# Kernel tuning notes

Hardware: AMD Instinct MI355X
Metric: run time of the kernel (lower is better)

## Reference

```python
import jax, jax.numpy as jnp
import numpy as np
import math

B, T, H, L, N = 8, 256, 1024, 6, 16
S = 3 * T          # interleaved (rtg, state, action) tokens
D = H // N
STATE_DIM, ACT_DIM, MAX_TSTEP, FF = 1024, 64, 4096, 4 * H
EPS = 1e-5


def _ln(x, g, b):
    m = jnp.mean(x, axis=-1, keepdims=True)
    v = jnp.var(x, axis=-1, keepdims=True)
    return (x - m) * jax.lax.rsqrt(v + EPS) * g + b


def setup_inputs() -> dict:
    key = jax.random.key(0)
    ks = jax.random.split(key, 32)
    sc = 0.02
    inp = {
        'timesteps': jax.random.randint(ks[0], (B, T), 0, MAX_TSTEP),
        'states': jax.random.randint(ks[1], (B, T), 0, STATE_DIM),
        'actions': jax.random.randint(ks[2], (B, T), 0, ACT_DIM),
        'returns_to_go': jax.random.normal(ks[3], (B, T, 1), jnp.float32),
        # embeddings
        'Wt': jax.random.normal(ks[4], (MAX_TSTEP, H), jnp.float32) * sc,
        'Ws': jax.random.normal(ks[5], (STATE_DIM, H), jnp.float32) * sc,
        'Wa': jax.random.normal(ks[6], (ACT_DIM, H), jnp.float32) * sc,
        'Wr': jax.random.normal(ks[7], (1, H), jnp.float32) * sc,
        'br': jnp.zeros((H,), jnp.float32),
        'lng': jnp.ones((H,), jnp.float32), 'lnb': jnp.zeros((H,), jnp.float32),
        # per-layer stacked params (weights stored [in,out]: y = x @ W + b)
        'Wq': jax.random.normal(ks[8], (L, H, H), jnp.float32) * sc,
        'bq': jnp.zeros((L, H), jnp.float32),
        'Wk': jax.random.normal(ks[9], (L, H, H), jnp.float32) * sc,
        'bk': jnp.zeros((L, H), jnp.float32),
        'Wv': jax.random.normal(ks[10], (L, H, H), jnp.float32) * sc,
        'bv': jnp.zeros((L, H), jnp.float32),
        'Wp': jax.random.normal(ks[11], (L, H, H), jnp.float32) * sc,
        'bp': jnp.zeros((L, H), jnp.float32),
        'W1': jax.random.normal(ks[12], (L, H, FF), jnp.float32) * sc,
        'b1': jnp.zeros((L, FF), jnp.float32),
        'W2': jax.random.normal(ks[13], (L, FF, H), jnp.float32) * sc,
        'b2': jnp.zeros((L, H), jnp.float32),
        'ln1g': jnp.ones((L, H), jnp.float32), 'ln1b': jnp.zeros((L, H), jnp.float32),
        'ln2g': jnp.ones((L, H), jnp.float32), 'ln2b': jnp.zeros((L, H), jnp.float32),
        # heads
        'Wrtg': jax.random.normal(ks[14], (H, 1), jnp.float32) * sc,
        'brtg': jnp.zeros((1,), jnp.float32),
        'Wst': jax.random.normal(ks[15], (H, STATE_DIM), jnp.float32) * sc,
        'bst': jnp.zeros((STATE_DIM,), jnp.float32),
        'Wac': jax.random.normal(ks[16], (H, ACT_DIM), jnp.float32) * sc,
        'bac': jnp.zeros((ACT_DIM,), jnp.float32),
    }
    return inp


def _attn(x, Wq, bq, Wk, bk, Wv, bv, Wp, bp, mask):
    q = (x @ Wq + bq).reshape(B, S, N, D)
    k = (x @ Wk + bk).reshape(B, S, N, D)
    v = (x @ Wv + bv).reshape(B, S, N, D)
    scores = jnp.einsum('bqhd,bkhd->bhqk', q, k) / math.sqrt(D)
    scores = jnp.where(mask, scores, -jnp.inf)
    p = jax.nn.softmax(scores, axis=-1)
    o = jnp.einsum('bhqk,bkhd->bqhd', p, v).reshape(B, S, H)
    return o @ Wp + bp


def _forward(timesteps, states, actions, returns_to_go, Wt, Ws, Wa, Wr, br,
             lng, lnb, Wq, bq, Wk, bk, Wv, bv, Wp, bp, W1, b1, W2, b2,
             ln1g, ln1b, ln2g, ln2b, Wrtg, brtg, Wst, bst, Wac, bac):
    te = Wt[timesteps]                         # [B,T,H]
    se = Ws[states] + te
    ae = Wa[actions] + te
    re = returns_to_go @ Wr + br + te
    # stack(dim=1).permute(0,2,1,3).reshape -> interleave (rtg, state, action)
    h = jnp.stack([re, se, ae], axis=2).reshape(B, S, H)
    h = _ln(h, lng, lnb)
    mask = jnp.tril(jnp.ones((S, S), bool))[None, None]
    for l in range(L):
        h = h + _attn(h, Wq[l], bq[l], Wk[l], bk[l], Wv[l], bv[l], Wp[l], bp[l], mask)
        h = _ln(h, ln1g[l], ln1b[l])
        h = h + (jax.nn.gelu(h @ W1[l] + b1[l], approximate=False) @ W2[l] + b2[l])
        h = _ln(h, ln2g[l], ln2b[l])
    h = h.reshape(B, 3, T, H)                  # as in the source (contiguous chunks)
    rtg_preds = h[:, 2] @ Wrtg + brtg
    state_preds = h[:, 2] @ Wst + bst
    action_preds = h[:, 1] @ Wac + bac         # discrete actions -> no tanh
    return (state_preds, action_preds, rtg_preds)


def reference(timesteps, states, actions, returns_to_go, Wt, Ws, Wa, Wr, br,
              lng, lnb, Wq, bq, Wk, bk, Wv, bv, Wp, bp, W1, b1, W2, b2,
              ln1g, ln1b, ln2g, ln2b, Wrtg, brtg, Wst, bst, Wac, bac):
    return _forward(timesteps, states, actions, returns_to_go, Wt, Ws, Wa, Wr, br,
                    lng, lnb, Wq, bq, Wk, bk, Wv, bv, Wp, bp, W1, b1, W2, b2,
                    ln1g, ln1b, ln2g, ln2b, Wrtg, brtg, Wst, bst, Wac, bac)
```

## Files before the change

### kernel.cpp

```cpp
#include <hip/hip_runtime.h>
#include <hip/hip_bf16.h>

#define DI __device__ __forceinline__

typedef unsigned short u16;
typedef __bf16 bf16x8 __attribute__((ext_vector_type(8)));
typedef unsigned short u16x8 __attribute__((ext_vector_type(8)));
typedef unsigned short u16x4 __attribute__((ext_vector_type(4)));
typedef float f32x4 __attribute__((ext_vector_type(4)));

static constexpr int Bb = 8, Tt = 256, Hh = 1024, Ll = 6, NHd = 16, Dh = 64;
static constexpr int Ss = 3 * Tt;
static constexpr int FFd = 4096;
static constexpr int BSr = Bb * Ss;
static constexpr int QKVld = 3072;

DI u16 f2bf(float f) {
  unsigned u = __builtin_bit_cast(unsigned, f);
  u += 0x7fffu + ((u >> 16) & 1u);
  return (u16)(u >> 16);
}

DI void gload_lds16(const u16* g, u16* l) {
  __builtin_amdgcn_global_load_lds((__attribute__((address_space(1))) void*)(g),
                                   (__attribute__((address_space(3))) void*)(l), 16, 0, 0);
}
DI bf16x8 ldl8(const u16* p) { return __builtin_bit_cast(bf16x8, *(const u16x8*)p); }
DI bf16x8 ldg8(const u16* p) { return __builtin_bit_cast(bf16x8, *(const u16x8*)p); }

DI void barRaw() {
  asm volatile("" ::: "memory");
  __builtin_amdgcn_s_barrier();
  asm volatile("" ::: "memory");
}

__global__ __launch_bounds__(256, 3) void gemm_db(
    const u16* __restrict__ A, const u16* __restrict__ Bt,
    const float* __restrict__ bias, const float* __restrict__ bias2,
    const float* __restrict__ bias3,
    float* __restrict__ outf, u16* __restrict__ outb,
    int Kstride, int Ksub, int ldc, int act, size_t psz)
{
  __shared__ u16 SM[24576];
  const int lane = threadIdx.x & 63, w = threadIdx.x >> 6;
  const int wr = w >> 1, wc = w & 1;
  const int l15 = lane & 15, l4 = lane >> 4;

  const int gx = gridDim.x, gy = gridDim.y, nwg = gx * gy;
  int f = blockIdx.y * gx + blockIdx.x;
  { int q = nwg >> 3, rr = nwg & 7, x = f & 7, idx = f >> 3;
    f = (x < rr ? x * (q + 1) : rr * (q + 1) + (x - rr) * q) + idx; }
  const int r2 = f % (gy * 8), cg = f / (gy * 8);
  const int bm = r2 >> 3, bn = cg * 8 + (r2 & 7);
  const int koff = blockIdx.z * Ksub;
  const int NT = Ksub >> 5;

  const int srow = lane >> 2;
  const int schunk = (((lane & 3) ^ ((srow >> 1) & 3)) << 3);
  unsigned aoff[2], boff[2];
#pragma unroll
  for (int i = 0; i < 2; ++i) {
    const int r = w * 32 + i * 16 + srow;
    aoff[i] = (unsigned)(bm * 128 + r) * (unsigned)Kstride + koff + schunk;
    boff[i] = (unsigned)(bn * 128 + r) * (unsigned)Kstride + koff + schunk;
  }

  auto stage = [&](int bsel, int kt) {
#pragma unroll
    for (int i = 0; i < 2; ++i) {
      gload_lds16(A + aoff[i] + kt * 32, &SM[bsel * 4096 + (w * 32 + i * 16) * 32]);
      gload_lds16(Bt + boff[i] + kt * 32, &SM[12288 + bsel * 4096 + (w * 32 + i * 16) * 32]);
    }
  };

  f32x4 acc[4][4] = {};

  stage(0, 0);
  stage(1, 1);
  asm volatile("s_waitcnt vmcnt(4)" ::: "memory");
  barRaw();

  const int ck = ((l4 ^ ((l15 >> 1) & 3)) << 3);
  int cur = 0;
  for (int t = 0; t < NT; ++t) {
    const int nxt = (cur + 2 >= 3) ? cur - 1 : cur + 2;
    if (t + 2 < NT) stage(nxt, t + 2);

    bf16x8 af[4], bf[4];
#pragma unroll
    for (int m = 0; m < 4; ++m)
      af[m] = ldl8(&SM[cur * 4096 + (wr * 64 + m * 16 + l15) * 32 + ck]);
#pragma unroll
    for (int n = 0; n < 4; ++n)
      bf[n] = ldl8(&SM[12288 + cur * 4096 + (wc * 64 + n * 16 + l15) * 32 + ck]);

    __builtin_amdgcn_s_setprio(1);
#pragma unroll
    for (int m = 0; m < 4; ++m)
#pragma unroll
      for (int n = 0; n < 4; ++n)
        acc[m][n] = __builtin_amdgcn_mfma_f32_16x16x32_bf16(af[m], bf[n], acc[m][n], 0, 0, 0);
    __builtin_amdgcn_s_setprio(0);

    if (t + 2 < NT)      asm volatile("s_waitcnt vmcnt(4)" ::: "memory");
    else if (t + 1 < NT) asm volatile("s_waitcnt vmcnt(0)" ::: "memory");
    barRaw();
    cur = (cur + 1 >= 3) ? 0 : cur + 1;
  }

  if (outb) {
#pragma unroll
    for (int n = 0; n < 4; ++n) {
      const int col = wc * 64 + n * 16 + l15;
      const int gcol = bn * 128 + col;
      float bval = 0.f;
      if (bias) {
        const float* bp_ = bias;
        int idx = gcol;
        if (bias2 && gcol >= 1024) { bp_ = (gcol >= 2048) ? bias3 : bias2; idx = gcol & 1023; }
        bval = bp_[idx];
      }
#pragma unroll
      for (int m = 0; m < 4; ++m) {
#pragma unroll
        for (int r = 0; r < 4; ++r) {
          const int lrow = wr * 64 + m * 16 + l4 * 4 + r;
          float x = acc[m][n][r] + bval;
          if (act) x = 0.5f * x * (1.f + erff(x * 0.70710678118654752f));
          SM[lrow * 128 + col] = f2bf(x);
        }
      }
    }
    barRaw();
#pragma unroll 4
    for (int rr2 = 0; rr2 < 32; ++rr2) {
      const int row = rr2 * 4 + w;
      *(unsigned*)&outb[(size_t)(bm * 128 + row) * ldc + bn * 128 + lane * 2] =
          *(const unsigned*)&SM[row * 128 + lane * 2];
    }
  } else if (outf) {
    float* Cf = (float*)SM;
#pragma unroll
    for (int half = 0; half < 2; ++half) {
      barRaw();
      if (wr == half) {
#pragma unroll
        for (int n = 0; n < 4; ++n) {
          const int col = wc * 64 + n * 16 + l15;
          const int gcol = bn * 128 + col;
          float bval = 0.f;
          if (bias) {
            const float* bp_ = bias;
            int idx = gcol;
            if (bias2 && gcol >= 1024) { bp_ = (gcol >= 2048) ? bias3 : bias2; idx = gcol & 1023; }
            bval = bp_[idx];
          }
#pragma unroll
          for (int m = 0; m < 4; ++m) {
#pragma unroll
            for (int r = 0; r < 4; ++r) {
              float x = acc[m][n][r] + bval;
              if (act) x = 0.5f * x * (1.f + erff(x * 0.70710678118654752f));
              Cf[(m * 16 + l4 * 4 + r) * 128 + col] = x;
            }
          }
        }
      }
      barRaw();
#pragma unroll 4
      for (int rr2 = 0; rr2 < 16; ++rr2) {
        const int row = rr2 * 4 + w;
        *(float2*)&outf[blockIdx.z * psz +
                        (size_t)(bm * 128 + half * 64 + row) * ldc + bn * 128 + lane * 2] =
            *(const float2*)&Cf[row * 128 + lane * 2];
      }
    }
  }
}

__global__ __launch_bounds__(256, 2) void gemm_bf16(
    const u16* __restrict__ A, const u16* __restrict__ Bt,
    const float* __restrict__ bias, float* __restrict__ outf,
    int M, int N, int K, int ldc, int Nstore, int rowmode, int rowoff)
{
  __shared__ u16 As[128 * 64];
  __shared__ u16 Bs[128 * 64];
  const int tid = threadIdx.x;
  const int lane = tid & 63;
  const int w = tid >> 6;
  const int wr = w >> 1, wc = w & 1;
  const int bn = blockIdx.x, bm = blockIdx.y;
  const int l3 = lane >> 3, l7 = lane & 7, l15 = lane & 15, l4 = lane >> 4;

  f32x4 acc[4][4] = {};

  const int schunk = (l7 ^ l3) << 3;
  size_t aoff[4], boff[4];
#pragma unroll
  for (int i = 0; i < 4; ++i) {
    int r = bm * 128 + w * 32 + i * 8 + l3;
    int ar = rowmode ? ((r >> 8) * Ss + rowoff + (r & 255)) : r;
    aoff[i] = (size_t)ar * K + schunk;
    boff[i] = (size_t)(bn * 128 + w * 32 + i * 8 + l3) * K + schunk;
  }

  for (int kt = 0; kt < K; kt += 64) {
    __syncthreads();
#pragma unroll
    for (int i = 0; i < 4; ++i) {
      gload_lds16(A + aoff[i] + kt, &As[(w * 32 + i * 8) * 64]);
      gload_lds16(Bt + boff[i] + kt, &Bs[(w * 32 + i * 8) * 64]);
    }
    __syncthreads();

    bf16x8 af[4][2], bf[4][2];
#pragma unroll
    for (int m = 0; m < 4; ++m) {
#pragma unroll
      for (int kk = 0; kk < 2; ++kk) {
        const int slot = ((kk * 4 + l4) ^ l7) << 3;
        af[m][kk] = ldl8(&As[(wr * 64 + m * 16 + l15) * 64 + slot]);
        bf[m][kk] = ldl8(&Bs[(wc * 64 + m * 16 + l15) * 64 + slot]);
      }
    }
#pragma unroll
    for (int m = 0; m < 4; ++m)
#pragma unroll
      for (int n = 0; n < 4; ++n)
#pragma unroll
        for (int kk = 0; kk < 2; ++kk)
          acc[m][n] = __builtin_amdgcn_mfma_f32_16x16x32_bf16(af[m][kk], bf[n][kk], acc[m][n], 0, 0, 0);
  }

#pragma unroll
  for (int n = 0; n < 4; ++n) {
    const int col = bn * 128 + wc * 64 + n * 16 + l15;
    const bool cok = col < Nstore;
    const float bv = (cok && bias) ? bias[col] : 0.f;
#pragma unroll
    for (int m = 0; m < 4; ++m) {
#pragma unroll
      for (int r = 0; r < 4; ++r) {
        const int row = bm * 128 + wr * 64 + m * 16 + l4 * 4 + r;
        if (cok) outf[(size_t)row * ldc + col] = acc[m][n][r] + bv;
      }
    }
  }
}

__global__ __launch_bounds__(256, 3) void attn_flash(
    const u16* __restrict__ qkv, const u16* __restrict__ vt, u16* __restrict__ o)
{
  __shared__ u16 Kl[2][64 * 64];
  __shared__ u16 Vl[2][64 * 64];
  __shared__ u16 Pl[4][16 * 64];
  const int qt = blockIdx.x, h = blockIdx.y, b = blockIdx.z;
  const int lane = threadIdx.x & 63, w = threadIdx.x >> 6;
  const int l15 = lane & 15, l4 = lane >> 4;

  const size_t qoff = (size_t)(b * Ss + qt * 64 + w * 16 + l15) * QKVld + h * Dh + l4 * 8;
  const bf16x8 aq0 = ldg8(qkv + qoff), aq1 = ldg8(qkv + qoff + 32);

  const u16* kg = qkv + (size_t)b * Ss * QKVld + 1024 + h * Dh;
  const u16* vg = vt + (size_t)(b * NHd + h) * Dh * Ss;

  int srow[2], scs[2];
#pragma unroll
  for (int i = 0; i < 2; ++i) {
    srow[i] = (w * 2 + i) * 8 + (lane >> 3);
    scs[i] = ((lane & 7) ^ (srow[i] & 7)) * 8;
  }

  float m[4] = {-1e30f, -1e30f, -1e30f, -1e30f};
  float lsum[4] = {0.f, 0.f, 0.f, 0.f};
  f32x4 oa[4] = {};

  auto stage = [&](int bsel, int kb) {
#pragma unroll
    for (int i = 0; i < 2; ++i) {
      gload_lds16(kg + (size_t)(kb * 64 + srow[i]) * QKVld + scs[i], &Kl[bsel][(w * 2 + i) * 8 * 64]);
      gload_lds16(vg + (size_t)srow[i] * Ss + kb * 64 + scs[i], &Vl[bsel][(w * 2 + i) * 8 * 64]);
    }
  };

  stage(0, 0);
  __syncthreads();
  int buf = 0;
  for (int kb = 0; kb <= qt; ++kb) {
    if (kb < qt) stage(buf ^ 1, kb + 1);

    f32x4 sc[4];
    __builtin_amdgcn_s_setprio(1);
#pragma unroll
    for (int fj = 0; fj < 4; ++fj) {
      const u16* kp = &Kl[buf][(fj * 16 + l15) * 64];
      const int r7 = l15 & 7;
      bf16x8 kf0 = ldl8(kp + ((l4 ^ r7) << 3));
      bf16x8 kf1 = ldl8(kp + (((4 + l4) ^ r7) << 3));
      f32x4 zz = {};
      zz = __builtin_amdgcn_mfma_f32_16x16x32_bf16(aq0, kf0, zz, 0, 0, 0);
      sc[fj] = __builtin_amdgcn_mfma_f32_16x16x32_bf16(aq1, kf1, zz, 0, 0, 0);
    }
    __builtin_amdgcn_s_setprio(0);

    float pm[4] = {-1e30f, -1e30f, -1e30f, -1e30f};
    const bool diag = (kb == qt);
#pragma unroll
    for (int fj = 0; fj < 4; ++fj)
#pragma unroll
      for (int r = 0; r < 4; ++r) {
        float s = sc[fj][r] * 0.125f;
        if (diag && (fj * 16 + l15) > (w * 16 + l4 * 4 + r)) s = -1e30f;
        sc[fj][r] = s;
        pm[r] = fmaxf(pm[r], s);
      }
#pragma unroll
    for (int d = 1; d < 16; d <<= 1)
#pragma unroll
      for (int r = 0; r < 4; ++r) pm[r] = fmaxf(pm[r], __shfl_xor(pm[r], d));

    float al[4], ps[4];
#pragma unroll
    for (int r = 0; r < 4; ++r) {
      float mn = fmaxf(m[r], pm[r]);
      al[r] = __expf(m[r] - mn);
      m[r] = mn;
      ps[r] = 0.f;
    }
#pragma unroll
    for (int fj = 0; fj < 4; ++fj)
#pragma unroll
      for (int r = 0; r < 4; ++r) {
        float p = __expf(sc[fj][r] - m[r]);
        sc[fj][r] = p;
        ps[r] += p;
      }
#pragma unroll
    for (int d = 1; d < 16; d <<= 1)
#pragma unroll
      for (int r = 0; r < 4; ++r) ps[r] += __shfl_xor(ps[r], d);
#pragma unroll
    for (int r = 0; r < 4; ++r) lsum[r] = lsum[r] * al[r] + ps[r];
#pragma unroll
    for (int fn = 0; fn < 4; ++fn)
#pragma unroll
      for (int r = 0; r < 4; ++r) oa[fn][r] *= al[r];

#pragma unroll
    for (int fj = 0; fj < 4; ++fj)
#pragma unroll
      for (int r = 0; r < 4; ++r) {
        const int key = fj * 16 + l15, qloc = l4 * 4 + r;
        Pl[w][qloc * 64 + (((key >> 3) ^ (qloc & 7)) << 3) + (key & 7)] = f2bf(sc[fj][r]);
      }

    const int q7 = l15 & 7;
    bf16x8 pa0 = ldl8(&Pl[w][l15 * 64 + ((l4 ^ q7) << 3)]);
    bf16x8 pa1 = ldl8(&Pl[w][l15 * 64 + (((4 + l4) ^ q7) << 3)]);
    __builtin_amdgcn_s_setprio(1);
#pragma unroll
    for (int fn = 0; fn < 4; ++fn) {
      const u16* vp = &Vl[buf][(fn * 16 + l15) * 64];
      bf16x8 vf0 = ldl8(vp + ((l4 ^ q7) << 3));
      bf16x8 vf1 = ldl8(vp + (((4 + l4) ^ q7) << 3));
      oa[fn] = __builtin_amdgcn_mfma_f32_16x16x32_bf16(pa0, vf0, oa[fn], 0, 0, 0);
      oa[fn] = __builtin_amdgcn_mfma_f32_16x16x32_bf16(pa1, vf1, oa[fn], 0, 0, 0);
    }
    __builtin_amdgcn_s_setprio(0);
    __syncthreads();
    buf ^= 1;
  }

#pragma unroll
  for (int fn = 0; fn < 4; ++fn)
#pragma unroll
    for (int r = 0; r < 4; ++r) {
      const int row = b * Ss + qt * 64 + w * 16 + l4 * 4 + r;
      o[(size_t)row * Hh + h * Dh + fn * 16 + l15] = f2bf(oa[fn][r] / lsum[r]);
    }
}

__global__ __launch_bounds__(256) void embed_ln(
    const int* __restrict__ timesteps, const int* __restrict__ states,
    const int* __restrict__ actions, const float* __restrict__ rtg,
    const float* __restrict__ Wt, const float* __restrict__ Ws,
    const float* __restrict__ Wa, const float* __restrict__ Wr,
    const float* __restrict__ br, const float* __restrict__ lng,
    const float* __restrict__ lnb, float* __restrict__ hout, u16* __restrict__ xb)
{
  __shared__ float red[8];
  const int s = blockIdx.x;
  const int b = s / Ss, sl = s % Ss;
  const int tt = sl / 3, kind = sl % 3;
  const int bt = b * Tt + tt;
  const int e = threadIdx.x * 4;

  const float4 tv = *(const float4*)(Wt + (size_t)timesteps[bt] * Hh + e);
  float v[4];
  if (kind == 0) {
    const float rr = rtg[bt];
    const float4 w4 = *(const float4*)(Wr + e);
    const float4 b4 = *(const float4*)(br + e);
    v[0] = rr * w4.x + b4.x + tv.x; v[1] = rr * w4.y + b4.y + tv.y;
    v[2] = rr * w4.z + b4.z + tv.z; v[3] = rr * w4.w + b4.w + tv.w;
  } else {
    const float* emb = (kind == 1) ? (Ws + (size_t)states[bt] * Hh)
                                   : (Wa + (size_t)actions[bt] * Hh);
    const float4 e4 = *(const float4*)(emb + e);
    v[0] = e4.x + tv.x; v[1] = e4.y + tv.y; v[2] = e4.z + tv.z; v[3] = e4.w + tv.w;
  }
  float s1 = v[0] + v[1] + v[2] + v[3];
  float s2 = v[0]*v[0] + v[1]*v[1] + v[2]*v[2] + v[3]*v[3];
#pragma unroll
  for (int d = 32; d; d >>= 1) { s1 += __shfl_xor(s1, d); s2 += __shfl_xor(s2, d); }
  if ((threadIdx.x & 63) == 0) { red[threadIdx.x >> 6] = s1; red[4 + (threadIdx.x >> 6)] = s2; }
  __syncthreads();
  s1 = red[0] + red[1] + red[2] + red[3];
  s2 = red[4] + red[5] + red[6] + red[7];
  const float mean = s1 * (1.f / 1024.f);
  const float var = s2 * (1.f / 1024.f) - mean * mean;
  const float rs = rsqrtf(var + 1e-5f);
  const float4 g4 = *(const float4*)(lng + e);
  const float4 bb4 = *(const float4*)(lnb + e);
  float o0 = (v[0] - mean) * rs * g4.x + bb4.x;
  float o1 = (v[1] - mean) * rs * g4.y + bb4.y;
  float o2 = (v[2] - mean) * rs * g4.z + bb4.z;
  float o3 = (v[3] - mean) * rs * g4.w + bb4.w;
  *(float4*)(hout + (size_t)s * Hh + e) = make_float4(o0, o1, o2, o3);
  u16x4 ov = {f2bf(o0), f2bf(o1), f2bf(o2), f2bf(o3)};
  *(u16x4*)(xb + (size_t)s * Hh + e) = ov;
}

__global__ __launch_bounds__(256) void ln_kernel(
    const float* __restrict__ inA, const float* __restrict__ inB,
    const float* __restrict__ resid, const float* __restrict__ bias,
    const float* __restrict__ g, const float* __restrict__ bta,
    float* __restrict__ hout, u16* __restrict__ xb)
{
  __shared__ float red[8];
  const int row = blockIdx.x;
  const int e = threadIdx.x * 4;
  const float4 a4 = *(const float4*)(inA + (size_t)row * Hh + e);
  float v[4] = {a4.x, a4.y, a4.z, a4.w};
  if (inB) {
    const float4 b4 = *(const float4*)(inB + (size_t)row * Hh + e);
    v[0] += b4.x; v[1] += b4.y; v[2] += b4.z; v[3] += b4.w;
  }
  if (resid) {
    const float4 r4 = *(const float4*)(resid + (size_t)row * Hh + e);
    v[0] += r4.x; v[1] += r4.y; v[2] += r4.z; v[3] += r4.w;
  }
  if (bias) {
    const float4 c4 = *(const float4*)(bias + e);
    v[0] += c4.x; v[1] += c4.y; v[2] += c4.z; v[3] += c4.w;
  }
  float s1 = v[0] + v[1] + v[2] + v[3];
  float s2 = v[0]*v[0] + v[1]*v[1] + v[2]*v[2] + v[3]*v[3];
#pragma unroll
  for (int d = 32; d; d >>= 1) { s1 += __shfl_xor(s1, d); s2 += __shfl_xor(s2, d); }
  if ((threadIdx.x & 63) == 0) { red[threadIdx.x >> 6] = s1; red[4 + (threadIdx.x >> 6)] = s2; }
  __syncthreads();
  s1 = red[0] + red[1] + red[2] + red[3];
  s2 = red[4] + red[5] + red[6] + red[7];
  const float mean = s1 * (1.f / 1024.f);
  const float var = s2 * (1.f / 1024.f) - mean * mean;
  const float rs = rsqrtf(var + 1e-5f);
  const float4 g4 = *(const float4*)(g + e);
  const float4 b4 = *(const float4*)(bta + e);
  float o0 = (v[0] - mean) * rs * g4.x + b4.x;
  float o1 = (v[1] - mean) * rs * g4.y + b4.y;
  float o2 = (v[2] - mean) * rs * g4.z + b4.z;
  float o3 = (v[3] - mean) * rs * g4.w + b4.w;
  *(float4*)(hout + (size_t)row * Hh + e) = make_float4(o0, o1, o2, o3);
  u16x4 ov = {f2bf(o0), f2bf(o1), f2bf(o2), f2bf(o3)};
  *(u16x4*)(xb + (size_t)row * Hh + e) = ov;
}

__global__ __launch_bounds__(256) void transpose_w(
    const float* __restrict__ W, u16* __restrict__ Wt, int Kd, int Nd, int Nout)
{
  __shared__ float tile[32][33];
  const int k0 = blockIdx.x * 32, n0 = blockIdx.y * 32;
  const int tx = threadIdx.x & 31, ty = threadIdx.x >> 5;
#pragma unroll
  for (int rr = 0; rr < 4; ++rr) {
    const int kk = ty + rr * 8;
    const int n = n0 + tx;
    tile[kk][tx] = (n < Nd) ? W[(size_t)(k0 + kk) * Nd + n] : 0.f;
  }
  __syncthreads();
#pragma unroll
  for (int rr = 0; rr < 4; ++rr) {
    Wt[(size_t)(n0 + ty + rr * 8) * Kd + k0 + tx] = f2bf(tile[tx][ty + rr * 8]);
  }
}

__global__ __launch_bounds__(256) void transpose_v(
    const u16* __restrict__ v, u16* __restrict__ vt)
{
  __shared__ u16 tile[64][72];
  const int s0 = blockIdx.x * 64, h = blockIdx.y, b = blockIdx.z;
  const int j8 = (threadIdx.x & 7) * 8;
#pragma unroll
  for (int half = 0; half < 2; ++half) {
    const int i = (threadIdx.x >> 3) + half * 32;
    *(u16x8*)&tile[i][j8] =
        *(const u16x8*)&v[(size_t)(b * Ss + s0 + i) * QKVld + 2048 + h * 64 + j8];
  }
  __syncthreads();
#pragma unroll
  for (int half = 0; half < 2; ++half) {
    const int d = (threadIdx.x >> 3) + half * 32;
    u16x8 ov;
#pragma unroll
    for (int ee = 0; ee < 8; ++ee) ov[ee] = tile[j8 + ee][d];
    *(u16x8*)&vt[((size_t)(b * NHd + h) * 64 + d) * Ss + s0 + j8] = ov;
  }
}

__global__ __launch_bounds__(256) void rtg_head(
    const float* __restrict__ h, const float* __restrict__ Wr1,
    const float* __restrict__ br1, float* __restrict__ out)
{
  const int lane = threadIdx.x & 63, w = threadIdx.x >> 6;
  const int row = blockIdx.x * 4 + w;
  const int b = row >> 8, tt = row & 255;
  const float* x = h + (size_t)(b * Ss + 512 + tt) * Hh;
  float s = 0.f;
  for (int e = lane; e < Hh; e += 64) s += x[e] * Wr1[e];
#pragma unroll
  for (int d = 32; d; d >>= 1) s += __shfl_xor(s, d);
  if (lane == 0) out[row] = s + br1[0];
}

extern "C" void kernel_launch(void* const* d_in, const int* in_sizes, int n_in,
                              void* d_out, int out_size, void* d_ws, size_t ws_size,
                              hipStream_t stream)
{
  (void)in_sizes; (void)n_in; (void)out_size; (void)ws_size;
  const int*   timesteps = (const int*)d_in[0];
  const int*   states    = (const int*)d_in[1];
  const int*   actions   = (const int*)d_in[2];
  const float* rtg       = (const float*)d_in[3];
  const float* Wt   = (const float*)d_in[4];
  const float* Ws   = (const float*)d_in[5];
  const float* Wa   = (const float*)d_in[6];
  const float* Wr   = (const float*)d_in[7];
  const float* br   = (const float*)d_in[8];
  const float* lng  = (const float*)d_in[9];
  const float* lnb  = (const float*)d_in[10];
  const float* Wq   = (const float*)d_in[11];
  const float* bq   = (const float*)d_in[12];
  const float* Wk   = (const float*)d_in[13];
  const float* bk   = (const float*)d_in[14];
  const float* Wv   = (const float*)d_in[15];
  const float* bv   = (const float*)d_in[16];
  const float* Wp   = (const float*)d_in[17];
  const float* bp   = (const float*)d_in[18];
  const float* W1   = (const float*)d_in[19];
  const float* b1   = (const float*)d_in[20];
  const float* W2   = (const float*)d_in[21];
  const float* b2   = (const float*)d_in[22];
  const float* ln1g = (const float*)d_in[23];
  const float* ln1b = (const float*)d_in[24];
  const float* ln2g = (const float*)d_in[25];
  const float* ln2b = (const float*)d_in[26];
  const float* Wrtg = (const float*)d_in[27];
  const float* brtg = (const float*)d_in[28];
  const float* Wst  = (const float*)d_in[29];
  const float* bst  = (const float*)d_in[30];
  const float* Wac  = (const float*)d_in[31];
  const float* bac  = (const float*)d_in[32];

  char* wp = (char*)d_ws;
  auto alloc = [&](size_t bytes) { void* p = wp; wp += (bytes + 511) & ~(size_t)511; return p; };
  float* hbuf = (float*)alloc((size_t)BSr * Hh * 4);
  float* p0   = (float*)alloc((size_t)BSr * Hh * 4);
  float* p1   = (float*)alloc((size_t)BSr * Hh * 4);
  u16* xb   = (u16*)alloc((size_t)BSr * Hh * 2);
  u16* qkvb = (u16*)alloc((size_t)BSr * QKVld * 2);
  u16* vtb  = (u16*)alloc((size_t)BSr * Hh * 2);
  u16* ob   = (u16*)alloc((size_t)BSr * Hh * 2);
  u16* ub   = (u16*)alloc((size_t)BSr * FFd * 2);
  u16* W3T  = (u16*)alloc((size_t)3 * Hh * Hh * 2);
  u16* WpT  = (u16*)alloc((size_t)Hh * Hh * 2);
  u16* W1T  = (u16*)alloc((size_t)FFd * Hh * 2);
  u16* W2T  = (u16*)alloc((size_t)Hh * FFd * 2);
  u16* WstT = (u16*)alloc((size_t)Hh * Hh * 2);
  u16* WacT = (u16*)alloc((size_t)128 * Hh * 2);

  float* out_state = (float*)d_out;
  float* out_act   = out_state + (size_t)2048 * 1024;
  float* out_rtg   = out_act + (size_t)2048 * 64;

  const size_t PSZ = (size_t)BSr * Hh;

  transpose_w<<<dim3(32, 32, 1), 256, 0, stream>>>(Wst, WstT, 1024, 1024, 1024);
  transpose_w<<<dim3(32, 4, 1), 256, 0, stream>>>(Wac, WacT, 1024, 64, 128);
  embed_ln<<<BSr, 256, 0, stream>>>(timesteps, states, actions, rtg, Wt, Ws, Wa, Wr,
                                    br, lng, lnb, hbuf, xb);

  for (int l = 0; l < Ll; ++l) {
    transpose_w<<<dim3(32, 32, 1), 256, 0, stream>>>(Wq + (size_t)l * Hh * Hh, W3T, 1024, 1024, 1024);
    transpose_w<<<dim3(32, 32, 1), 256, 0, stream>>>(Wk + (size_t)l * Hh * Hh, W3T + (size_t)Hh * Hh, 1024, 1024, 1024);
    transpose_w<<<dim3(32, 32, 1), 256, 0, stream>>>(Wv + (size_t)l * Hh * Hh, W3T + (size_t)2 * Hh * Hh, 1024, 1024, 1024);
    transpose_w<<<dim3(32, 32, 1), 256, 0, stream>>>(Wp + (size_t)l * Hh * Hh, WpT, 1024, 1024, 1024);
    transpose_w<<<dim3(32, 128, 1), 256, 0, stream>>>(W1 + (size_t)l * Hh * FFd, W1T, 1024, 4096, 4096);
    transpose_w<<<dim3(128, 32, 1), 256, 0, stream>>>(W2 + (size_t)l * FFd * Hh, W2T, 4096, 1024, 1024);

    gemm_db<<<dim3(24, 48, 1), 256, 0, stream>>>(
        xb, W3T, bq + l * Hh, bk + l * Hh, bv + l * Hh, nullptr, qkvb,
        Hh, Hh, QKVld, 0, 0);
    transpose_v<<<dim3(12, 16, 8), 256, 0, stream>>>(qkvb, vtb);
    attn_flash<<<dim3(12, 16, 8), 256, 0, stream>>>(qkvb, vtb, ob);
    gemm_db<<<dim3(8, 48, 2), 256, 0, stream>>>(
        ob, WpT, nullptr, nullptr, nullptr, p0, nullptr,
        Hh, 512, Hh, 0, PSZ);
    ln_kernel<<<BSr, 256, 0, stream>>>(p0, p1, hbuf, bp + l * Hh,
                                       ln1g + l * Hh, ln1b + l * Hh, hbuf, xb);
    gemm_db<<<dim3(32, 48, 1), 256, 0, stream>>>(
        xb, W1T, b1 + l * FFd, nullptr, nullptr, nullptr, ub,
        Hh, Hh, FFd, 1, 0);
    gemm_db<<<dim3(8, 48, 2), 256, 0, stream>>>(
        ub, W2T, nullptr, nullptr, nullptr, p0, nullptr,
        FFd, 2048, Hh, 0, PSZ);
    ln_kernel<<<BSr, 256, 0, stream>>>(p0, p1, hbuf, b2 + l * Hh,
                                       ln2g + l * Hh, ln2b + l * Hh, hbuf, xb);
  }

  gemm_bf16<<<dim3(8, 16), 256, 0, stream>>>(xb, WstT, bst, out_state,
                                             2048, 1024, 1024, 1024, 1024, 1, 512);
  gemm_bf16<<<dim3(1, 16), 256, 0, stream>>>(xb, WacT, bac, out_act,
                                             2048, 128, 1024, 64, 64, 1, 256);
  rtg_head<<<512, 256, 0, stream>>>(hbuf, Wrtg, brtg, out_rtg);
}
```

Baseline: 2.235 ms.

## Switch GEMM to BK=64 double buffering with 8-chunk XOR swizzle

Changes the GEMM K-tile from 32 to 64 and replaces the three-stage LDS ring with a two-stage double buffer. The LDS row swizzle is redone for 64-element rows, and launch bounds drop from 3 to 2 blocks per SM to fit the larger LDS footprint. The aim is to halve the number of barriers and loop iterations and raise MFMA work per sync. In exchange it loses a prefetch stage of latency hiding, waits on vmcnt(0) every iteration, and lowers occupancy.

```diff
diff --git a/kernel.cpp b/kernel.cpp
--- a/kernel.cpp
+++ b/kernel.cpp
@@ -34,14 +34,14 @@
   asm volatile("" ::: "memory");
 }
 
-__global__ __launch_bounds__(256, 3) void gemm_db(
+__global__ __launch_bounds__(256, 2) void gemm_db(
     const u16* __restrict__ A, const u16* __restrict__ Bt,
     const float* __restrict__ bias, const float* __restrict__ bias2,
     const float* __restrict__ bias3,
     float* __restrict__ outf, u16* __restrict__ outb,
     int Kstride, int Ksub, int ldc, int act, size_t psz)
 {
-  __shared__ u16 SM[24576];
+  __shared__ u16 SM[32768];
   const int lane = threadIdx.x & 63, w = threadIdx.x >> 6;
   const int wr = w >> 1, wc = w & 1;
   const int l15 = lane & 15, l4 = lane >> 4;
@@ -53,59 +53,62 @@
   const int r2 = f % (gy * 8), cg = f / (gy * 8);
   const int bm = r2 >> 3, bn = cg * 8 + (r2 & 7);
   const int koff = blockIdx.z * Ksub;
-  const int NT = Ksub >> 5;
-
-  const int srow = lane >> 2;
-  const int schunk = (((lane & 3) ^ ((srow >> 1) & 3)) << 3);
-  unsigned aoff[2], boff[2];
-#pragma unroll
-  for (int i = 0; i < 2; ++i) {
-    const int r = w * 32 + i * 16 + srow;
+  const int NT = Ksub >> 6;
+
+  const int srow = lane >> 3;
+  const int schunk = ((lane & 7) ^ srow) << 3;
+  unsigned aoff[4], boff[4];
+#pragma unroll
+  for (int i = 0; i < 4; ++i) {
+    const int r = w * 32 + i * 8 + srow;
     aoff[i] = (unsigned)(bm * 128 + r) * (unsigned)Kstride + koff + schunk;
     boff[i] = (unsigned)(bn * 128 + r) * (unsigned)Kstride + koff + schunk;
   }
 
   auto stage = [&](int bsel, int kt) {
 #pragma unroll
-    for (int i = 0; i < 2; ++i) {
-      gload_lds16(A + aoff[i] + kt * 32, &SM[bsel * 4096 + (w * 32 + i * 16) * 32]);
-      gload_lds16(Bt + boff[i] + kt * 32, &SM[12288 + bsel * 4096 + (w * 32 + i * 16) * 32]);
-    }
+    for (int i = 0; i < 4; ++i)
+      gload_lds16(A + aoff[i] + kt * 64, &SM[bsel * 8192 + (w * 32 + i * 8) * 64]);
+#pragma unroll
+    for (int i = 0; i < 4; ++i)
+      gload_lds16(Bt + boff[i] + kt * 64, &SM[16384 + bsel * 8192 + (w * 32 + i * 8) * 64]);
   };
 
   f32x4 acc[4][4] = {};
 
   stage(0, 0);
-  stage(1, 1);
-  asm volatile("s_waitcnt vmcnt(4)" ::: "memory");
+  asm volatile("s_waitcnt vmcnt(0)" ::: "memory");
   barRaw();
 
-  const int ck = ((l4 ^ ((l15 >> 1) & 3)) << 3);
+  const int r7 = l15 & 7;
   int cur = 0;
   for (int t = 0; t < NT; ++t) {
-    const int nxt = (cur + 2 >= 3) ? cur - 1 : cur + 2;
-    if (t + 2 < NT) stage(nxt, t + 2);
-
-    bf16x8 af[4], bf[4];
-#pragma unroll
-    for (int m = 0; m < 4; ++m)
-      af[m] = ldl8(&SM[cur * 4096 + (wr * 64 + m * 16 + l15) * 32 + ck]);
-#pragma unroll
-    for (int n = 0; n < 4; ++n)
-      bf[n] = ldl8(&SM[12288 + cur * 4096 + (wc * 64 + n * 16 + l15) * 32 + ck]);
+    if (t + 1 < NT) stage(cur ^ 1, t + 1);
+
+    bf16x8 af[4][2], bf[4][2];
+#pragma unroll
+    for (int m = 0; m < 4; ++m) {
+#pragma unroll
+      for (int kk = 0; kk < 2; ++kk) {
+        const int slot = (((kk * 4 + l4) ^ r7) << 3);
+        af[m][kk] = ldl8(&SM[cur * 8192 + (wr * 64 + m * 16 + l15) * 64 + slot]);
+        bf[m][kk] = ldl8(&SM[16384 + cur * 8192 + (wc * 64 + m * 16 + l15) * 64 + slot]);
+      }
+    }
 
     __builtin_amdgcn_s_setprio(1);
 #pragma unroll
-    for (int m = 0; m < 4; ++m)
-#pragma unroll
-      for (int n = 0; n < 4; ++n)
-        acc[m][n] = __builtin_amdgcn_mfma_f32_16x16x32_bf16(af[m], bf[n], acc[m][n], 0, 0, 0);
+    for (int kk = 0; kk < 2; ++kk)
+#pragma unroll
+      for (int m = 0; m < 4; ++m)
+#pragma unroll
+        for (int n = 0; n < 4; ++n)
+          acc[m][n] = __builtin_amdgcn_mfma_f32_16x16x32_bf16(af[m][kk], bf[n][kk], acc[m][n], 0, 0, 0);
     __builtin_amdgcn_s_setprio(0);
 
-    if (t + 2 < NT)      asm volatile("s_waitcnt vmcnt(4)" ::: "memory");
-    else if (t + 1 < NT) asm volatile("s_waitcnt vmcnt(0)" ::: "memory");
+    if (t + 1 < NT) asm volatile("s_waitcnt vmcnt(0)" ::: "memory");
     barRaw();
-    cur = (cur + 1 >= 3) ? 0 : cur + 1;
+    cur ^= 1;
   }
 
   if (outb) {
```

New measurement: 2.420 ms. 8.3% more time.
